# Kernel tuning notes

Measured on AMD Instinct MI355X. Metric: run time of the kernel, lower is better.

Reference implementation:

```python
import jax, jax.numpy as jnp
import numpy as np

D_MODEL = 1024
N_HEADS = 16
HEAD_DIM = D_MODEL // N_HEADS  # 64
BATCH, SEQ = 2, 2048
MASK_FILL = -1000000000.0


def setup_inputs() -> dict:
    key = jax.random.key(0)
    ks = jax.random.split(key, 13)
    s = 1.0 / np.sqrt(D_MODEL)
    inp = {
        "q": jax.random.normal(ks[0], (BATCH, SEQ, D_MODEL), jnp.float32),
        "k": jax.random.normal(ks[1], (BATCH, SEQ, D_MODEL), jnp.float32),
        "v": jax.random.normal(ks[2], (BATCH, SEQ, D_MODEL), jnp.float32),
        "mask": jax.random.randint(ks[3], (BATCH, 1, SEQ, SEQ), 0, 2, jnp.int32),
        "Wq": jax.random.normal(ks[4], (D_MODEL, D_MODEL), jnp.float32) * s,
        "bq": jax.random.normal(ks[5], (D_MODEL,), jnp.float32) * s,
        "Wk": jax.random.normal(ks[6], (D_MODEL, D_MODEL), jnp.float32) * s,
        "bk": jax.random.normal(ks[7], (D_MODEL,), jnp.float32) * s,
        "Wv": jax.random.normal(ks[8], (D_MODEL, D_MODEL), jnp.float32) * s,
        "bv": jax.random.normal(ks[9], (D_MODEL,), jnp.float32) * s,
        "Wo": jax.random.normal(ks[10], (D_MODEL, D_MODEL), jnp.float32) * s,
        "bo": jax.random.normal(ks[11], (D_MODEL,), jnp.float32) * s,
    }
    return inp


def reference(q, k, v, mask, Wq, bq, Wk, bk, Wv, bv, Wo, bo):
    batch, seq, feat = q.shape
    # Linear projections (torch Linear: x @ W.T + b)
    qp = q @ Wq.T + bq
    kp = k @ Wk.T + bk
    vp = v @ Wv.T + bv

    def split(x):
        # (B, S, D) -> (B, H, S, Dh)
        return x.reshape(batch, seq, N_HEADS, HEAD_DIM).swapaxes(1, 2)

    qh, kh, vh = split(qp), split(kp), split(vp)

    # (B, H, S, S) score matrix, scaled
    score = jnp.einsum("bhqd,bhkd->bhqk", qh, kh) / jnp.sqrt(
        jnp.asarray(HEAD_DIM, qh.dtype))
    score = jnp.where(mask == 0, jnp.asarray(MASK_FILL, score.dtype), score)
    attn = jax.nn.softmax(score, axis=-1)
    out = jnp.einsum("bhqk,bhkd->bhqd", attn, vh)  # (B, H, S, Dh)
    joint = out.swapaxes(1, 2).reshape(batch, seq, feat)
    return joint @ Wo.T + bo
```

## Files before the change

### kernel.cpp

```cpp
#include <hip/hip_runtime.h>

typedef unsigned short u16;
typedef unsigned long long u64;
typedef float f32x4 __attribute__((ext_vector_type(4)));
typedef __bf16 bf16x4 __attribute__((ext_vector_type(4)));
typedef __bf16 bf16x8 __attribute__((ext_vector_type(8)));
typedef u16 u16x8 __attribute__((ext_vector_type(8)));

#define QSCALE 0.18033688011112042f

__device__ __forceinline__ u16 f2bf(float f) {
  unsigned int u = __float_as_uint(f);
  u += 0x7fffu + ((u >> 16) & 1u);
  return (u16)(u >> 16);
}

__device__ __forceinline__ void async16(const void* g, void* l) {
  __builtin_amdgcn_global_load_lds(
      (__attribute__((address_space(1))) void*)g,
      (__attribute__((address_space(3))) void*)l,
      16, 0, 0);
}

__device__ __forceinline__ f32x4 mfma16(bf16x8 a, bf16x8 b, f32x4 c) {
  return __builtin_amdgcn_mfma_f32_16x16x32_bf16(a, b, c, 0, 0, 0);
}

struct CvtArgs {
  const float* src[7];
  u16* dst[7];
};

__global__ __launch_bounds__(256) void cvt_kernel(CvtArgs a) {
  int z = blockIdx.z;
  int n = (z < 3) ? 4194304 : 1048576;
  int base = (blockIdx.x * 256 + threadIdx.x) * 8;
  if (base >= n) return;
  const float* s = a.src[z] + base;
  f32x4 x0 = *(const f32x4*)s;
  f32x4 x1 = *(const f32x4*)(s + 4);
  u16x8 pk;
  pk[0]=f2bf(x0[0]); pk[1]=f2bf(x0[1]); pk[2]=f2bf(x0[2]); pk[3]=f2bf(x0[3]);
  pk[4]=f2bf(x1[0]); pk[5]=f2bf(x1[1]); pk[6]=f2bf(x1[2]); pk[7]=f2bf(x1[3]);
  *(u16x8*)(a.dst[z] + base) = pk;
}

__global__ __launch_bounds__(256) void pack_mask_kernel(
    const int* __restrict__ mask, u64* __restrict__ pm) {
  int idx = blockIdx.x * 256 + threadIdx.x;
  const int4* src = (const int4*)(mask + (size_t)idx * 64);
  u64 bits = 0ull;
#pragma unroll
  for (int j = 0; j < 16; ++j) {
    int4 v = src[j];
    if (v.x) bits |= 1ull << (4 * j + 0);
    if (v.y) bits |= 1ull << (4 * j + 1);
    if (v.z) bits |= 1ull << (4 * j + 2);
    if (v.w) bits |= 1ull << (4 * j + 3);
  }
  pm[idx] = bits;
}

__device__ __forceinline__ void gemm_body(const u16* __restrict__ A,
                                          const u16* __restrict__ W,
                                          const float* __restrict__ bias,
                                          void* __restrict__ outraw, int mode,
                                          float oscale) {
  alignas(16) __shared__ u16 lA[128 * 32];
  alignas(16) __shared__ u16 lB[128 * 32];
  const int tid = threadIdx.x;
  const int lane = tid & 63, wv = tid >> 6;
  const int wm = wv >> 1, wn = wv & 1;
  const int m0 = blockIdx.y * 128, n0 = blockIdx.x * 128;
  const int l15 = lane & 15, quad = lane >> 4;
  const int srow = lane >> 2;
  const int scol = (lane & 3) * 8;

  f32x4 acc[4][4] = {};

  for (int k0 = 0; k0 < 1024; k0 += 32) {
#pragma unroll
    for (int t = 0; t < 2; ++t) {
      int rb = (wv * 2 + t) * 16;
      async16(A + (size_t)(m0 + rb + srow) * 1024 + k0 + scol, (char*)lA + rb * 64);
      async16(W + (size_t)(n0 + rb + srow) * 1024 + k0 + scol, (char*)lB + rb * 64);
    }
    __syncthreads();
    bf16x8 af[4], bfr[4];
#pragma unroll
    for (int i = 0; i < 4; ++i) {
      af[i]  = *(const bf16x8*)(lA + (wm * 64 + i * 16 + l15) * 32 + quad * 8);
      bfr[i] = *(const bf16x8*)(lB + (wn * 64 + i * 16 + l15) * 32 + quad * 8);
    }
#pragma unroll
    for (int i = 0; i < 4; ++i)
#pragma unroll
      for (int j = 0; j < 4; ++j)
        acc[i][j] = mfma16(af[i], bfr[j], acc[i][j]);
    __syncthreads();
  }

#pragma unroll
  for (int i = 0; i < 4; ++i) {
    int mbase = m0 + wm * 64 + i * 16 + quad * 4;
#pragma unroll
    for (int j = 0; j < 4; ++j) {
      int n = n0 + wn * 64 + j * 16 + l15;
      float bv = bias[n];
#pragma unroll
      for (int r = 0; r < 4; ++r) {
        int m = mbase + r;
        float val = (acc[i][j][r] + bv) * oscale;
        if (mode == 0) {
          int b = m >> 11, s = m & 2047, h = n >> 6, dh = n & 63;
          ((u16*)outraw)[((((size_t)b * 16 + h) * 2048 + s) << 6) + dh] = f2bf(val);
        } else if (mode == 1) {
          int b = m >> 11, s = m & 2047, h = n >> 6, dh = n & 63;
          ((u16*)outraw)[((((size_t)b * 16 + h) * 64 + dh) << 11) + s] = f2bf(val);
        } else {
          ((float*)outraw)[(size_t)m * 1024 + n] = val;
        }
      }
    }
  }
}

__global__ __launch_bounds__(256) void gemm_qkv_kernel(
    const u16* __restrict__ qb, const u16* __restrict__ kb, const u16* __restrict__ vb,
    const u16* __restrict__ Wqb, const float* __restrict__ bq,
    const u16* __restrict__ Wkb, const float* __restrict__ bk,
    const u16* __restrict__ Wvb, const float* __restrict__ bv,
    u16* __restrict__ qp, u16* __restrict__ kp, u16* __restrict__ vt) {
  if (blockIdx.z == 0)      gemm_body(qb, Wqb, bq, qp, 0, QSCALE);
  else if (blockIdx.z == 1) gemm_body(kb, Wkb, bk, kp, 0, 1.0f);
  else                      gemm_body(vb, Wvb, bv, vt, 1, 1.0f);
}

__global__ __launch_bounds__(256) void gemm_o_kernel(
    const u16* __restrict__ joint, const u16* __restrict__ Wob,
    const float* __restrict__ bo, float* __restrict__ out) {
  gemm_body(joint, Wob, bo, out, 2, 1.0f);
}

__global__ __launch_bounds__(256, 2) void attn_kernel(
    const u16* __restrict__ qp, const u16* __restrict__ kp,
    const u16* __restrict__ vt, const u64* __restrict__ pm,
    u16* __restrict__ joint) {
  alignas(16) __shared__ u16 kbuf[2][4096];
  alignas(16) __shared__ u16 vbuf[2][4096];
  alignas(16) __shared__ u16 pbuf[4][2][1024];

  const int tid = threadIdx.x, lane = tid & 63, wv = tid >> 6;
  const int quad = lane >> 4, l15 = lane & 15;
  const int q0 = blockIdx.x * 128;
  const int h = blockIdx.y, b = blockIdx.z;
  const size_t head_off = ((size_t)b * 16 + h) * 2048 * 64;
  const u16* Qh = qp + head_off;
  const u16* Kh = kp + head_off;
  const u16* Vh = vt + head_off;
  const int qr0 = q0 + wv * 32 + l15;
  const u64* pmq = pm + ((size_t)b * 2048 + qr0) * 32;

  bf16x8 qf[2][2];
#pragma unroll
  for (int g = 0; g < 2; ++g) {
    const u16* qrow = Qh + (size_t)(qr0 + g * 16) * 64 + quad * 8;
    qf[g][0] = *(const bf16x8*)(qrow);
    qf[g][1] = *(const bf16x8*)(qrow + 32);
  }

  const int sd0 = tid, sd1 = 256 + tid;
  const int snt0 = sd0 >> 7, shalf0 = (sd0 >> 6) & 1, sl60 = sd0 & 63;
  const int snt1 = sd1 >> 7, shalf1 = (sd1 >> 6) & 1, sl61 = sd1 & 63;
  const u16* kg0 = Kh + (size_t)(snt0 * 16 + (sl60 & 15)) * 64 + shalf0 * 32 + (sl60 >> 4) * 8;
  const u16* kg1 = Kh + (size_t)(snt1 * 16 + (sl61 & 15)) * 64 + shalf1 * 32 + (sl61 >> 4) * 8;
  const int vb0 = sd0 >> 6, vb1 = sd1 >> 6;
  const u16* vg0 = Vh + (size_t)((vb0 >> 1) * 16 + (sl60 & 15)) * 2048 + (vb0 & 1) * 32 + (sl60 >> 4) * 8;
  const u16* vg1 = Vh + (size_t)((vb1 >> 1) * 16 + (sl61 & 15)) * 2048 + (vb1 & 1) * 32 + (sl61 >> 4) * 8;

  f32x4 O[2][4] = {};
  f32x4 lacc[2] = {};

  async16(kg0, (char*)kbuf[0] + sd0 * 16);
  async16(kg1, (char*)kbuf[0] + sd1 * 16);
  async16(vg0, (char*)vbuf[0] + sd0 * 16);
  async16(vg1, (char*)vbuf[0] + sd1 * 16);

  for (int kt = 0; kt < 32; ++kt) {
    __syncthreads();

    if (kt != 31) {
      const size_t kadv = (size_t)(kt + 1) * 4096;
      const int vadv = (kt + 1) * 64;
      char* kd = (char*)kbuf[(kt + 1) & 1];
      char* vd = (char*)vbuf[(kt + 1) & 1];
      async16(kg0 + kadv, kd + sd0 * 16);
      async16(kg1 + kadv, kd + sd1 * 16);
      async16(vg0 + vadv, vd + sd0 * 16);
      async16(vg1 + vadv, vd + sd1 * 16);
    }

    u64 w0 = pmq[kt], w1 = pmq[kt + 512];
    const u16* kc = kbuf[kt & 1];
    const u16* vc = vbuf[kt & 1];

    bf16x8 kf[8];
#pragma unroll
    for (int nt = 0; nt < 4; ++nt) {
      kf[2 * nt]     = *(const bf16x8*)(kc + nt * 1024 + lane * 8);
      kf[2 * nt + 1] = *(const bf16x8*)(kc + nt * 1024 + 512 + lane * 8);
    }

    f32x4 S[2][4];
#pragma unroll
    for (int g = 0; g < 2; ++g)
#pragma unroll
      for (int nt = 0; nt < 4; ++nt) {
        f32x4 z = {};
        z = mfma16(kf[2 * nt], qf[g][0], z);
        S[g][nt] = mfma16(kf[2 * nt + 1], qf[g][1], z);
      }

#pragma unroll
    for (int g = 0; g < 2; ++g) {
      u64 word = g ? w1 : w0;
      unsigned int wlo = (unsigned int)word, whi = (unsigned int)(word >> 32);
#pragma unroll
      for (int nt = 0; nt < 4; ++nt) {
        unsigned int hw = (nt < 2) ? wlo : whi;
        unsigned int nib = hw >> ((nt & 1) * 16 + quad * 4);
#pragma unroll
        for (int r = 0; r < 4; ++r) {
          float pe = __builtin_amdgcn_exp2f(S[g][nt][r]);
          S[g][nt][r] = ((nib >> r) & 1u) ? pe : 0.f;
        }
        lacc[g] += S[g][nt];
        bf16x4 pv = __builtin_convertvector(S[g][nt], bf16x4);
        int t4 = 4 * nt + quad;
        int ks = t4 >> 3, qd = (t4 & 7) >> 1;
        u16* pw = pbuf[wv][g] + ks * 512 + qd * 128 + l15 * 8 + (t4 & 1) * 4;
        *(u64*)pw = *(const u64*)&pv;
      }
    }

    bf16x8 vf[8];
#pragma unroll
    for (int nt = 0; nt < 4; ++nt) {
      vf[2 * nt]     = *(const bf16x8*)(vc + (nt * 2) * 512 + lane * 8);
      vf[2 * nt + 1] = *(const bf16x8*)(vc + (nt * 2 + 1) * 512 + lane * 8);
    }
    asm volatile("s_waitcnt lgkmcnt(0)" ::: "memory");

#pragma unroll
    for (int ks = 0; ks < 2; ++ks) {
      bf16x8 pf0 = *(const bf16x8*)(pbuf[wv][0] + ks * 512 + lane * 8);
      bf16x8 pf1 = *(const bf16x8*)(pbuf[wv][1] + ks * 512 + lane * 8);
#pragma unroll
      for (int nt = 0; nt < 4; ++nt) {
        O[0][nt] = mfma16(vf[2 * nt + ks], pf0, O[0][nt]);
        O[1][nt] = mfma16(vf[2 * nt + ks], pf1, O[1][nt]);
      }
    }
  }

#pragma unroll
  for (int g = 0; g < 2; ++g) {
    float l = (lacc[g][0] + lacc[g][1]) + (lacc[g][2] + lacc[g][3]);
    l += __shfl_xor(l, 16, 64);
    l += __shfl_xor(l, 32, 64);
    float inv = 1.0f / l;
    size_t row_off = ((size_t)b * 2048 + qr0 + g * 16) * 1024 + h * 64;
#pragma unroll
    for (int nt = 0; nt < 4; ++nt) {
      f32x4 ov = O[g][nt] * inv;
      bf16x4 obv = __builtin_convertvector(ov, bf16x4);
      *(u64*)(joint + row_off + nt * 16 + quad * 4) = *(const u64*)&obv;
    }
  }
}

extern "C" void kernel_launch(void* const* d_in, const int* in_sizes, int n_in,
                              void* d_out, int out_size, void* d_ws, size_t ws_size,
                              hipStream_t stream) {
  const float* q  = (const float*)d_in[0];
  const float* k  = (const float*)d_in[1];
  const float* v  = (const float*)d_in[2];
  const int* mask = (const int*)d_in[3];
  const float* Wq = (const float*)d_in[4];
  const float* bq = (const float*)d_in[5];
  const float* Wk = (const float*)d_in[6];
  const float* bk = (const float*)d_in[7];
  const float* Wv = (const float*)d_in[8];
  const float* bv = (const float*)d_in[9];
  const float* Wo = (const float*)d_in[10];
  const float* bo = (const float*)d_in[11];
  float* out = (float*)d_out;

  u16* w = (u16*)d_ws;
  u16* qp    = w;
  u16* kp    = w + 4194304;
  u16* vt    = w + 8388608;
  u16* qb    = w + 12582912;
  u16* kb    = w + 16777216;
  u16* vb    = w + 20971520;
  u16* Wqb   = w + 25165824;
  u16* Wkb   = w + 26214400;
  u16* Wvb   = w + 27262976;
  u16* Wob   = w + 28311552;
  u64* pm    = (u64*)(w + 29360128);
  u16* joint = qb;

  CvtArgs ca;
  ca.src[0] = q;  ca.dst[0] = qb;
  ca.src[1] = k;  ca.dst[1] = kb;
  ca.src[2] = v;  ca.dst[2] = vb;
  ca.src[3] = Wq; ca.dst[3] = Wqb;
  ca.src[4] = Wk; ca.dst[4] = Wkb;
  ca.src[5] = Wv; ca.dst[5] = Wvb;
  ca.src[6] = Wo; ca.dst[6] = Wob;

  pack_mask_kernel<<<dim3(512), dim3(256), 0, stream>>>(mask, pm);
  cvt_kernel<<<dim3(2048, 1, 7), dim3(256), 0, stream>>>(ca);
  gemm_qkv_kernel<<<dim3(8, 32, 3), dim3(256), 0, stream>>>(
      qb, kb, vb, Wqb, bq, Wkb, bk, Wvb, bv, qp, kp, vt);
  attn_kernel<<<dim3(16, 16, 2), dim3(256), 0, stream>>>(qp, kp, vt, pm, joint);
  gemm_o_kernel<<<dim3(8, 32, 1), dim3(256), 0, stream>>>(joint, Wob, bo, out);
}
```

Baseline: 286.0 us.

## Split attention and output GEMM along K with atomic accumulation and separate normalize

Attention blocks now each process half of the key tiles and atomically accumulate unnormalized O and row sums into fp32 buffers, with a new kernel normalizing and converting to bf16. The output projection is split along K into two halves that atomically add into a zeroed output. Mask packing is folded into the conversion launch and the attention kernel's occupancy hint is raised. This adds parallelism and fewer launches at the cost of large atomic traffic, extra memsets and an extra normalization pass.

```diff
diff --git a/kernel.cpp b/kernel.cpp
--- a/kernel.cpp
+++ b/kernel.cpp
@@ -29,43 +29,46 @@
 struct CvtArgs {
   const float* src[7];
   u16* dst[7];
+  const int* mask;
+  u64* pm;
 };
 
 __global__ __launch_bounds__(256) void cvt_kernel(CvtArgs a) {
   int z = blockIdx.z;
-  int n = (z < 3) ? 4194304 : 1048576;
-  int base = (blockIdx.x * 256 + threadIdx.x) * 8;
-  if (base >= n) return;
-  const float* s = a.src[z] + base;
-  f32x4 x0 = *(const f32x4*)s;
-  f32x4 x1 = *(const f32x4*)(s + 4);
-  u16x8 pk;
-  pk[0]=f2bf(x0[0]); pk[1]=f2bf(x0[1]); pk[2]=f2bf(x0[2]); pk[3]=f2bf(x0[3]);
-  pk[4]=f2bf(x1[0]); pk[5]=f2bf(x1[1]); pk[6]=f2bf(x1[2]); pk[7]=f2bf(x1[3]);
-  *(u16x8*)(a.dst[z] + base) = pk;
-}
-
-__global__ __launch_bounds__(256) void pack_mask_kernel(
-    const int* __restrict__ mask, u64* __restrict__ pm) {
-  int idx = blockIdx.x * 256 + threadIdx.x;
-  const int4* src = (const int4*)(mask + (size_t)idx * 64);
-  u64 bits = 0ull;
-#pragma unroll
-  for (int j = 0; j < 16; ++j) {
-    int4 v = src[j];
-    if (v.x) bits |= 1ull << (4 * j + 0);
-    if (v.y) bits |= 1ull << (4 * j + 1);
-    if (v.z) bits |= 1ull << (4 * j + 2);
-    if (v.w) bits |= 1ull << (4 * j + 3);
-  }
-  pm[idx] = bits;
+  int tid0 = blockIdx.x * 256 + threadIdx.x;
+  if (z < 7) {
+    int n = (z < 3) ? 4194304 : 1048576;
+    int base = tid0 * 8;
+    if (base >= n) return;
+    const float* s = a.src[z] + base;
+    f32x4 x0 = *(const f32x4*)s;
+    f32x4 x1 = *(const f32x4*)(s + 4);
+    u16x8 pk;
+    pk[0]=f2bf(x0[0]); pk[1]=f2bf(x0[1]); pk[2]=f2bf(x0[2]); pk[3]=f2bf(x0[3]);
+    pk[4]=f2bf(x1[0]); pk[5]=f2bf(x1[1]); pk[6]=f2bf(x1[2]); pk[7]=f2bf(x1[3]);
+    *(u16x8*)(a.dst[z] + base) = pk;
+  } else {
+    if (tid0 >= 131072) return;
+    const int4* src = (const int4*)(a.mask + (size_t)tid0 * 64);
+    u64 bits = 0ull;
+#pragma unroll
+    for (int j = 0; j < 16; ++j) {
+      int4 v = src[j];
+      if (v.x) bits |= 1ull << (4 * j + 0);
+      if (v.y) bits |= 1ull << (4 * j + 1);
+      if (v.z) bits |= 1ull << (4 * j + 2);
+      if (v.w) bits |= 1ull << (4 * j + 3);
+    }
+    a.pm[tid0] = bits;
+  }
 }
 
 __device__ __forceinline__ void gemm_body(const u16* __restrict__ A,
                                           const u16* __restrict__ W,
                                           const float* __restrict__ bias,
                                           void* __restrict__ outraw, int mode,
-                                          float oscale) {
+                                          float oscale, int kbeg, int kend,
+                                          float bscale) {
   alignas(16) __shared__ u16 lA[128 * 32];
   alignas(16) __shared__ u16 lB[128 * 32];
   const int tid = threadIdx.x;
@@ -78,7 +81,7 @@
 
   f32x4 acc[4][4] = {};
 
-  for (int k0 = 0; k0 < 1024; k0 += 32) {
+  for (int k0 = kbeg; k0 < kend; k0 += 32) {
 #pragma unroll
     for (int t = 0; t < 2; ++t) {
       int rb = (wv * 2 + t) * 16;
@@ -106,7 +109,7 @@
 #pragma unroll
     for (int j = 0; j < 4; ++j) {
       int n = n0 + wn * 64 + j * 16 + l15;
-      float bv = bias[n];
+      float bv = bias[n] * bscale;
 #pragma unroll
       for (int r = 0; r < 4; ++r) {
         int m = mbase + r;
@@ -118,7 +121,7 @@
           int b = m >> 11, s = m & 2047, h = n >> 6, dh = n & 63;
           ((u16*)outraw)[((((size_t)b * 16 + h) * 64 + dh) << 11) + s] = f2bf(val);
         } else {
-          ((float*)outraw)[(size_t)m * 1024 + n] = val;
+          unsafeAtomicAdd(&((float*)outraw)[(size_t)m * 1024 + n], val);
         }
       }
     }
@@ -131,21 +134,22 @@
     const u16* __restrict__ Wkb, const float* __restrict__ bk,
     const u16* __restrict__ Wvb, const float* __restrict__ bv,
     u16* __restrict__ qp, u16* __restrict__ kp, u16* __restrict__ vt) {
-  if (blockIdx.z == 0)      gemm_body(qb, Wqb, bq, qp, 0, QSCALE);
-  else if (blockIdx.z == 1) gemm_body(kb, Wkb, bk, kp, 0, 1.0f);
-  else                      gemm_body(vb, Wvb, bv, vt, 1, 1.0f);
+  if (blockIdx.z == 0)      gemm_body(qb, Wqb, bq, qp, 0, QSCALE, 0, 1024, 1.0f);
+  else if (blockIdx.z == 1) gemm_body(kb, Wkb, bk, kp, 0, 1.0f, 0, 1024, 1.0f);
+  else                      gemm_body(vb, Wvb, bv, vt, 1, 1.0f, 0, 1024, 1.0f);
 }
 
 __global__ __launch_bounds__(256) void gemm_o_kernel(
     const u16* __restrict__ joint, const u16* __restrict__ Wob,
     const float* __restrict__ bo, float* __restrict__ out) {
-  gemm_body(joint, Wob, bo, out, 2, 1.0f);
-}
-
-__global__ __launch_bounds__(256, 2) void attn_kernel(
+  int z = blockIdx.z;
+  gemm_body(joint, Wob, bo, out, 2, 1.0f, z * 512, z * 512 + 512, z ? 0.0f : 1.0f);
+}
+
+__global__ __launch_bounds__(256, 3) void attn_kernel(
     const u16* __restrict__ qp, const u16* __restrict__ kp,
     const u16* __restrict__ vt, const u64* __restrict__ pm,
-    u16* __restrict__ joint) {
+    float* __restrict__ O_acc, float* __restrict__ l_acc) {
   alignas(16) __shared__ u16 kbuf[2][4096];
   alignas(16) __shared__ u16 vbuf[2][4096];
   alignas(16) __shared__ u16 pbuf[4][2][1024];
@@ -153,7 +157,9 @@
   const int tid = threadIdx.x, lane = tid & 63, wv = tid >> 6;
   const int quad = lane >> 4, l15 = lane & 15;
   const int q0 = blockIdx.x * 128;
-  const int h = blockIdx.y, b = blockIdx.z;
+  const int h = blockIdx.y;
+  const int b = blockIdx.z >> 1, sp = blockIdx.z & 1;
+  const int kt0 = sp * 16, kt1 = kt0 + 16;
   const size_t head_off = ((size_t)b * 16 + h) * 2048 * 64;
   const u16* Qh = qp + head_off;
   const u16* Kh = kp + head_off;
@@ -181,15 +187,19 @@
   f32x4 O[2][4] = {};
   f32x4 lacc[2] = {};
 
-  async16(kg0, (char*)kbuf[0] + sd0 * 16);
-  async16(kg1, (char*)kbuf[0] + sd1 * 16);
-  async16(vg0, (char*)vbuf[0] + sd0 * 16);
-  async16(vg1, (char*)vbuf[0] + sd1 * 16);
-
-  for (int kt = 0; kt < 32; ++kt) {
+  {
+    const size_t kadv = (size_t)kt0 * 4096;
+    const int vadv = kt0 * 64;
+    async16(kg0 + kadv, (char*)kbuf[0] + sd0 * 16);
+    async16(kg1 + kadv, (char*)kbuf[0] + sd1 * 16);
+    async16(vg0 + vadv, (char*)vbuf[0] + sd0 * 16);
+    async16(vg1 + vadv, (char*)vbuf[0] + sd1 * 16);
+  }
+
+  for (int kt = kt0; kt < kt1; ++kt) {
     __syncthreads();
 
-    if (kt != 31) {
+    if (kt != kt1 - 1) {
       const size_t kadv = (size_t)(kt + 1) * 4096;
       const int vadv = (kt + 1) * 64;
       char* kd = (char*)kbuf[(kt + 1) & 1];
@@ -263,20 +273,43 @@
     }
   }
 
+  float lsum[2];
 #pragma unroll
   for (int g = 0; g < 2; ++g) {
     float l = (lacc[g][0] + lacc[g][1]) + (lacc[g][2] + lacc[g][3]);
     l += __shfl_xor(l, 16, 64);
     l += __shfl_xor(l, 32, 64);
-    float inv = 1.0f / l;
-    size_t row_off = ((size_t)b * 2048 + qr0 + g * 16) * 1024 + h * 64;
-#pragma unroll
-    for (int nt = 0; nt < 4; ++nt) {
-      f32x4 ov = O[g][nt] * inv;
-      bf16x4 obv = __builtin_convertvector(ov, bf16x4);
-      *(u64*)(joint + row_off + nt * 16 + quad * 4) = *(const u64*)&obv;
-    }
-  }
+    lsum[g] = l;
+  }
+  size_t obase = (((size_t)b * 16 + h) * 2048 + qr0) * 64;
+#pragma unroll
+  for (int g = 0; g < 2; ++g)
+#pragma unroll
+    for (int nt = 0; nt < 4; ++nt)
+#pragma unroll
+      for (int r = 0; r < 4; ++r)
+        unsafeAtomicAdd(O_acc + obase + (size_t)g * 1024 + nt * 16 + quad * 4 + r,
+                        O[g][nt][r]);
+  if (quad == 0) {
+    size_t lbase = ((size_t)b * 16 + h) * 2048 + qr0;
+    unsafeAtomicAdd(l_acc + lbase, lsum[0]);
+    unsafeAtomicAdd(l_acc + lbase + 16, lsum[1]);
+  }
+}
+
+__global__ __launch_bounds__(256) void norm_kernel(
+    const float* __restrict__ O_acc, const float* __restrict__ l_acc,
+    u16* __restrict__ joint) {
+  int idx = blockIdx.x * 256 + threadIdx.x;
+  int row = idx >> 3, c = idx & 7;
+  float inv = 1.0f / l_acc[row];
+  const f32x4* src = (const f32x4*)(O_acc + (size_t)idx * 8);
+  f32x4 a = src[0] * inv, d = src[1] * inv;
+  int b = row >> 15, h = (row >> 11) & 15, q = row & 2047;
+  u16x8 pk;
+  pk[0]=f2bf(a[0]); pk[1]=f2bf(a[1]); pk[2]=f2bf(a[2]); pk[3]=f2bf(a[3]);
+  pk[4]=f2bf(d[0]); pk[5]=f2bf(d[1]); pk[6]=f2bf(d[2]); pk[7]=f2bf(d[3]);
+  *(u16x8*)(joint + ((size_t)(b * 2048 + q)) * 1024 + h * 64 + c * 8) = pk;
 }
 
 extern "C" void kernel_launch(void* const* d_in, const int* in_sizes, int n_in,
@@ -309,6 +342,8 @@
   u16* Wob   = w + 28311552;
   u64* pm    = (u64*)(w + 29360128);
   u16* joint = qb;
+  float* O_acc = (float*)(w + 16777216);
+  float* l_acc = (float*)(w + 25165824);
 
   CvtArgs ca;
   ca.src[0] = q;  ca.dst[0] = qb;
@@ -318,11 +353,14 @@
   ca.src[4] = Wk; ca.dst[4] = Wkb;
   ca.src[5] = Wv; ca.dst[5] = Wvb;
   ca.src[6] = Wo; ca.dst[6] = Wob;
-
-  pack_mask_kernel<<<dim3(512), dim3(256), 0, stream>>>(mask, pm);
-  cvt_kernel<<<dim3(2048, 1, 7), dim3(256), 0, stream>>>(ca);
+  ca.mask = mask; ca.pm = pm;
+
+  hipMemsetAsync(d_out, 0, (size_t)out_size * 4, stream);
+  cvt_kernel<<<dim3(2048, 1, 8), dim3(256), 0, stream>>>(ca);
   gemm_qkv_kernel<<<dim3(8, 32, 3), dim3(256), 0, stream>>>(
       qb, kb, vb, Wqb, bq, Wkb, bk, Wvb, bv, qp, kp, vt);
-  attn_kernel<<<dim3(16, 16, 2), dim3(256), 0, stream>>>(qp, kp, vt, pm, joint);
-  gemm_o_kernel<<<dim3(8, 32, 1), dim3(256), 0, stream>>>(joint, Wob, bo, out);
-}
+  hipMemsetAsync((void*)(w + 16777216), 0, (size_t)17039360, stream);
+  attn_kernel<<<dim3(16, 16, 4), dim3(256), 0, stream>>>(qp, kp, vt, pm, O_acc, l_acc);
+  norm_kernel<<<dim3(2048), dim3(256), 0, stream>>>(O_acc, l_acc, joint);
+  gemm_o_kernel<<<dim3(8, 32, 2), dim3(256), 0, stream>>>(joint, Wob, bo, out);
+}
```

New measurement: 413.5 us. +44.6%, slower.
